# Performance work log

Hardware: AMD Instinct MI355X
Metric: run time of the kernel (lower is better)

The kernel has to match this reference:

```python
import jax, jax.numpy as jnp
import numpy as np

B, S, LC, DIM, H, FFN = 1, 3600, 512, 1536, 12, 8960
HD = DIM // H          # 128
GRID = (4, 30, 30)     # f*h*w == S
K_LEN = 9900           # hardcoded k_lens in SelfAttention.forward
EPS = 1e-6

def _rope_axis_angles(n_pos, dim):
    inv = 1.0 / np.power(10000.0, np.arange(0, dim, 2, dtype=np.float64) / dim)
    return np.outer(np.arange(n_pos), inv)

def _build_rope(grid, head_dim):
    c = head_dim // 2                      # 64
    c1, c2 = c - 2 * (c // 3), c // 3      # 22, 21 (Wan 3D rope split)
    f, h, w = grid
    af = _rope_axis_angles(f, 2 * c1)
    ah = _rope_axis_angles(h, 2 * c2)
    aw = _rope_axis_angles(w, 2 * c2)
    ang = np.concatenate([
        np.broadcast_to(af[:, None, None, :], (f, h, w, c1)),
        np.broadcast_to(ah[None, :, None, :], (f, h, w, c2)),
        np.broadcast_to(aw[None, None, :, :], (f, h, w, c2)),
    ], axis=-1).reshape(f * h * w, c)
    return np.cos(ang).astype(np.float32), np.sin(ang).astype(np.float32)

def setup_inputs():
    key = jax.random.key(0)
    ks = iter(jax.random.split(key, 40))
    cos, sin = _build_rope(GRID, HD)
    inp = {
        'x': jax.random.normal(next(ks), (B, S, DIM), dtype=jnp.float32),
        'context': jax.random.normal(next(ks), (B, LC, DIM), dtype=jnp.float32),
        't_mod': 0.1 * jax.random.normal(next(ks), (B, 6, DIM), dtype=jnp.float32),
        'rope_cos': jnp.asarray(cos), 'rope_sin': jnp.asarray(sin),
        'modulation': jax.random.normal(next(ks), (1, 6, DIM), dtype=jnp.float32) / DIM ** 0.5,
    }
    for p in ('sa', 'ca'):
        for w in ('q', 'k', 'v', 'o'):
            inp[p + '_' + w + 'w'] = 0.02 * jax.random.normal(next(ks), (DIM, DIM), dtype=jnp.float32)
            inp[p + '_' + w + 'b'] = jnp.zeros((DIM,), jnp.float32)
        inp[p + '_nq'] = jnp.ones((DIM,), jnp.float32)
        inp[p + '_nk'] = jnp.ones((DIM,), jnp.float32)
    inp['n3_w'] = jnp.ones((DIM,), jnp.float32)
    inp['n3_b'] = jnp.zeros((DIM,), jnp.float32)
    inp['ffn_w1'] = 0.02 * jax.random.normal(next(ks), (DIM, FFN), dtype=jnp.float32)
    inp['ffn_b1'] = jnp.zeros((FFN,), jnp.float32)
    inp['ffn_w2'] = 0.02 * jax.random.normal(next(ks), (FFN, DIM), dtype=jnp.float32)
    inp['ffn_b2'] = jnp.zeros((DIM,), jnp.float32)
    return inp

def _rms(x, w):
    x32 = x.astype(jnp.float32)
    n = x32 * jax.lax.rsqrt(jnp.mean(x32 * x32, axis=-1, keepdims=True) + EPS)
    return n.astype(x.dtype) * w

def _ln(x, w=None, b=None):
    mu = jnp.mean(x, axis=-1, keepdims=True)
    var = jnp.mean(jnp.square(x - mu), axis=-1, keepdims=True)
    y = (x - mu) * jax.lax.rsqrt(var + EPS)
    return y if w is None else y * w + b

def _rope(x, cos, sin):
    b, s, h, d = x.shape
    x2 = x.reshape(b, s, h, d // 2, 2)
    xe, xo = x2[..., 0], x2[..., 1]
    c, sn = cos[None, :, None, :], sin[None, :, None, :]
    return jnp.stack([xe * c - xo * sn, xe * sn + xo * c], axis=-1).reshape(b, s, h, d)

def _attn(q, k, v, k_len=None):
    # q,k,v: [B,S,H,D]
    scores = jnp.einsum('bqhd,bkhd->bhqk', q, k) * (q.shape[-1] ** -0.5)
    if k_len is not None:
        mask = jnp.arange(k.shape[1]) < k_len
        scores = jnp.where(mask[None, None, None, :], scores, jnp.finfo(scores.dtype).min)
    return jnp.einsum('bhqk,bkhd->bqhd', jax.nn.softmax(scores, axis=-1), v)

def reference(x, context, t_mod, rope_cos, rope_sin, modulation,
              sa_qw, sa_qb, sa_kw, sa_kb, sa_vw, sa_vb, sa_ow, sa_ob, sa_nq, sa_nk,
              ca_qw, ca_qb, ca_kw, ca_kb, ca_vw, ca_vb, ca_ow, ca_ob, ca_nq, ca_nk,
              n3_w, n3_b, ffn_w1, ffn_b1, ffn_w2, ffn_b2):
    mod = modulation + t_mod                      # [B,6,DIM]
    sh_msa, sc_msa, g_msa, sh_mlp, sc_mlp, g_mlp = [mod[:, i:i + 1] for i in range(6)]
    b = x.shape[0]
    # --- self-attention with AdaLN modulate + 3D RoPE + k_lens mask ---
    h = _ln(x) * (1 + sc_msa) + sh_msa
    q = _rms(h @ sa_qw + sa_qb, sa_nq).reshape(b, -1, H, HD)
    k = _rms(h @ sa_kw + sa_kb, sa_nk).reshape(b, -1, H, HD)
    v = (h @ sa_vw + sa_vb).reshape(b, -1, H, HD)
    a = _attn(_rope(q, rope_cos, rope_sin), _rope(k, rope_cos, rope_sin), v, k_len=K_LEN)
    x = x + g_msa * (a.reshape(b, -1, DIM) @ sa_ow + sa_ob)
    # --- cross-attention ---
    hc = _ln(x, n3_w, n3_b)
    q = _rms(hc @ ca_qw + ca_qb, ca_nq).reshape(b, -1, H, HD)
    k = _rms(context @ ca_kw + ca_kb, ca_nk).reshape(b, -1, H, HD)
    v = (context @ ca_vw + ca_vb).reshape(b, -1, H, HD)
    x = x + (_attn(q, k, v).reshape(b, -1, DIM) @ ca_ow + ca_ob)
    # --- gated FFN with AdaLN modulate ---
    h = _ln(x) * (1 + sc_mlp) + sh_mlp
    h = jax.nn.gelu(h @ ffn_w1 + ffn_b1, approximate=True) @ ffn_w2 + ffn_b2
    return x + g_mlp * h
```

## Files before the change

kernel.cpp:

```cpp
#include <hip/hip_runtime.h>
#include <cstdint>

#define S_LEN 3600
#define DMODEL 1536
#define LCTX 512
#define NH 12
#define HDIM 128
#define FFND 8960
#define SPAD_SELF 3648

typedef short v8s __attribute__((ext_vector_type(8)));
typedef float v4f __attribute__((ext_vector_type(4)));
typedef unsigned short u16b;
typedef unsigned int u32b;

#define AS1 __attribute__((address_space(1)))
#define AS3 __attribute__((address_space(3)))

__device__ __forceinline__ void gl_lds16(const void* g, void* l){
  __builtin_amdgcn_global_load_lds((AS1 const void*)g, (AS3 void*)l, 16, 0, 0);
}

__device__ __forceinline__ u16b f2b(float f){
  union { float f; u32b i; } x; x.f = f;
  u32b r = x.i + 0x7fffu + ((x.i >> 16) & 1u);
  return (u16b)(r >> 16);
}

__device__ __forceinline__ u32b cvtpk(float a, float b){
  u32b r;
  asm("v_cvt_pk_bf16_f32 %0, %1, %2" : "=v"(r) : "v"(a), "v"(b));
  return r;
}

__device__ __forceinline__ int swz4(int row){ return (row ^ (row >> 2)) & 3; }

__global__ void add_vec(const float* __restrict__ a, const float* __restrict__ b,
                        float* __restrict__ o, int n){
  int i = blockIdx.x * 256 + threadIdx.x;
  if (i < n) o[i] = a[i] + b[i];
}

__global__ void f2b_kernel(const float* __restrict__ in, u16b* __restrict__ out, int n){
  int i = blockIdx.x * 256 + threadIdx.x;
  if (i < n) out[i] = f2b(in[i]);
}

struct WJob { const float* W; u16b* WT; int K; int N; int t0; };
struct WJobs { WJob j[10]; };

__global__ __launch_bounds__(256) void wconv(WJobs jobs){
  __shared__ float tile[32][33];
  int b = blockIdx.x;
  int ji = 0;
  #pragma unroll
  for (int i = 0; i < 10; ++i) if (b >= jobs.j[i].t0) ji = i;
  WJob jb = jobs.j[ji];
  int rel = b - jb.t0;
  int ntn = jb.N / 32;
  int k0 = (rel / ntn) * 32, n0 = (rel % ntn) * 32;
  int tx = threadIdx.x & 31, ty = threadIdx.x >> 5;
  #pragma unroll
  for (int r = ty; r < 32; r += 8) tile[r][tx] = jb.W[(size_t)(k0 + r) * jb.N + n0 + tx];
  __syncthreads();
  #pragma unroll
  for (int r = ty; r < 32; r += 8) jb.WT[(size_t)(n0 + r) * jb.K + k0 + tx] = f2b(tile[tx][r]);
}

__global__ __launch_bounds__(256) void vtrans(const u16b* __restrict__ V,
                                              u16b* __restrict__ Vt,
                                              int S, int Spad){
  __shared__ u16b t[32][136];
  int h = blockIdx.y, kb = blockIdx.x * 32, tid = threadIdx.x;
  int row = tid >> 3, ch = tid & 7;
  int key = kb + row;
  if (key < S){
    float4 a = *(const float4*)(V + (size_t)key * DMODEL + h * HDIM + ch * 16);
    float4 b = *(const float4*)(V + (size_t)key * DMODEL + h * HDIM + ch * 16 + 8);
    *(float4*)&t[row][ch * 16] = a;
    *(float4*)&t[row][ch * 16 + 8] = b;
  } else {
    float4 z = {0.f, 0.f, 0.f, 0.f};
    *(float4*)&t[row][ch * 16] = z;
    *(float4*)&t[row][ch * 16 + 8] = z;
  }
  __syncthreads();
  int hd = tid >> 1, kc = (tid & 1) * 16;
  u16b* dst = Vt + ((size_t)h * HDIM + hd) * Spad + kb + kc;
  #pragma unroll
  for (int e = 0; e < 16; e += 2){
    u32b pk = ((u32b)t[kc + e][hd]) | (((u32b)t[kc + e + 1][hd]) << 16);
    *(u32b*)(dst + e) = pk;
  }
}

__global__ __launch_bounds__(256) void ln_mod(const float* __restrict__ X,
                                              const float* __restrict__ gamma,
                                              const float* __restrict__ beta,
                                              float gadd, u16b* __restrict__ out){
  int row = blockIdx.x;
  const float* xr = X + (size_t)row * DMODEL;
  int tid = threadIdx.x;
  float v[6]; float s1 = 0.f, s2 = 0.f;
  #pragma unroll
  for (int j = 0; j < 6; ++j){ v[j] = xr[tid + j * 256]; s1 += v[j]; s2 += v[j] * v[j]; }
  #pragma unroll
  for (int o = 1; o < 64; o <<= 1){ s1 += __shfl_xor(s1, o); s2 += __shfl_xor(s2, o); }
  __shared__ float red[8];
  int wid = tid >> 6, lane = tid & 63;
  if (!lane){ red[wid * 2] = s1; red[wid * 2 + 1] = s2; }
  __syncthreads();
  s1 = red[0] + red[2] + red[4] + red[6];
  s2 = red[1] + red[3] + red[5] + red[7];
  float mu = s1 / DMODEL;
  float var = s2 / DMODEL - mu * mu;
  float rstd = rsqrtf(var + 1e-6f);
  #pragma unroll
  for (int j = 0; j < 6; ++j){
    int c = tid + j * 256;
    float g = gamma[c] + gadd;
    float b = beta[c];
    out[(size_t)row * DMODEL + c] = f2b((v[j] - mu) * rstd * g + b);
  }
}

__global__ __launch_bounds__(256) void rms_rope(const float* __restrict__ X,
                                                const float* __restrict__ w,
                                                const float* __restrict__ cosT,
                                                const float* __restrict__ sinT,
                                                float qmul,
                                                u16b* __restrict__ out){
  int row = blockIdx.x;
  const float* xr = X + (size_t)row * DMODEL;
  int tid = threadIdx.x;
  float2 v[3]; float ss = 0.f;
  #pragma unroll
  for (int j = 0; j < 3; ++j){
    v[j] = *(const float2*)(xr + 2 * (tid + j * 256));
    ss += v[j].x * v[j].x + v[j].y * v[j].y;
  }
  #pragma unroll
  for (int o = 1; o < 64; o <<= 1) ss += __shfl_xor(ss, o);
  __shared__ float red[4];
  int wid = tid >> 6, lane = tid & 63;
  if (!lane) red[wid] = ss;
  __syncthreads();
  ss = red[0] + red[1] + red[2] + red[3];
  float rstd = rsqrtf(ss / DMODEL + 1e-6f);
  #pragma unroll
  for (int j = 0; j < 3; ++j){
    int p = tid + j * 256;
    float xe = v[j].x * rstd * w[2 * p];
    float xo = v[j].y * rstd * w[2 * p + 1];
    float oe, oo;
    if (cosT){
      int d = p & 63;
      float c = cosT[row * 64 + d], sn = sinT[row * 64 + d];
      oe = xe * c - xo * sn; oo = xe * sn + xo * c;
    } else { oe = xe; oo = xo; }
    oe *= qmul; oo *= qmul;
    u32b packed = ((u32b)f2b(oe)) | (((u32b)f2b(oo)) << 16);
    *(u32b*)(out + (size_t)row * DMODEL + 2 * p) = packed;
  }
}

template<int EPI>
__global__ __launch_bounds__(256, 2) void gemm_bt(
    const u16b* __restrict__ A, const u16b* __restrict__ BT,
    const float* __restrict__ bias, const float* __restrict__ res,
    const float* __restrict__ gate, float* __restrict__ outF,
    u16b* __restrict__ outB, int M, int N, int K, int kLen)
{
  __shared__ char Asm[2][8192];
  __shared__ char Bsm[2][8192];
  const int tid = threadIdx.x, lane = tid & 63, wid = tid >> 6;
  const int bm = blockIdx.x * 128, bn = blockIdx.y * 128;
  const int kbase = blockIdx.z * kLen;
  const int wm = (wid >> 1) * 64, wn = (wid & 1) * 64;
  v4f acc[4][4] = {};

  auto stage = [&](int buf, int k0){
    #pragma unroll
    for (int c = 0; c < 2; ++c){
      int seg = wid * 2 + c;
      int l = seg * 64 + lane;
      int row = l >> 2, cs = l & 3;
      int col = cs ^ swz4(row);
      gl_lds16(A + (size_t)min(bm + row, M - 1) * K + kbase + k0 + col * 8,
               Asm[buf] + seg * 1024);
      gl_lds16(BT + (size_t)(bn + row) * K + kbase + k0 + col * 8,
               Bsm[buf] + seg * 1024);
    }
  };

  const int nt = kLen / 32;
  int cur = 0;
  stage(0, 0);
  __syncthreads();
  const int chk = lane >> 4, qr = lane & 15;
  for (int t = 0; t < nt; ++t){
    if (t + 1 < nt) stage(cur ^ 1, (t + 1) * 32);
    char* Ab = Asm[cur]; char* Bb = Bsm[cur];
    v8s af[4], bfr[4];
    #pragma unroll
    for (int f = 0; f < 4; ++f){
      int rowa = wm + f * 16 + qr;
      af[f] = *(const v8s*)(Ab + rowa * 64 + ((chk ^ swz4(rowa)) * 16));
      int rowb = wn + f * 16 + qr;
      bfr[f] = *(const v8s*)(Bb + rowb * 64 + ((chk ^ swz4(rowb)) * 16));
    }
    __builtin_amdgcn_s_setprio(1);
    #pragma unroll
    for (int i = 0; i < 4; ++i)
      #pragma unroll
      for (int j = 0; j < 4; ++j)
        acc[i][j] = __builtin_amdgcn_mfma_f32_16x16x32_bf16(af[i], bfr[j], acc[i][j], 0, 0, 0);
    __builtin_amdgcn_s_setprio(0);
    __syncthreads();
    cur ^= 1;
  }
  const int rr = lane >> 4;
  #pragma unroll
  for (int i = 0; i < 4; ++i){
    #pragma unroll
    for (int j = 0; j < 4; ++j){
      int n = bn + wn + j * 16 + qr;
      float bv = (EPI != 5 && bias) ? bias[n] : 0.f;
      float gv = (EPI == 2 && gate) ? gate[n] : 1.f;
      #pragma unroll
      for (int r = 0; r < 4; ++r){
        int m = bm + wm + i * 16 + rr * 4 + r;
        if (m < M){
          float val = acc[i][j][r] + bv;
          size_t idx = (size_t)m * N + n;
          if (EPI == 0) outB[idx] = f2b(val);
          else if (EPI == 1) outF[idx] = val;
          else if (EPI == 2) outF[idx] = res[idx] + gv * val;
          else if (EPI == 5) outF[(size_t)blockIdx.z * M * N + idx] = val;
          else {
            float t3 = val * val * val;
            float th = tanhf(0.7978845608028654f * (val + 0.044715f * t3));
            outB[idx] = f2b(0.5f * val * (1.f + th));
          }
        }
      }
    }
  }
}

struct Seg { const float* bias; float* outF; u16b* outB; };
struct Segs { Seg s[3]; };

__global__ __launch_bounds__(256, 2) void gemm_seg(
    const u16b* __restrict__ A, const u16b* __restrict__ BT,
    Segs segs, int M, int N, int K)
{
  __shared__ char Asm[2][8192];
  __shared__ char Bsm[2][8192];
  const int tid = threadIdx.x, lane = tid & 63, wid = tid >> 6;
  const int bm = blockIdx.x * 128, bn = blockIdx.y * 128;
  const int wm = (wid >> 1) * 64, wn = (wid & 1) * 64;
  v4f acc[4][4] = {};

  auto stage = [&](int buf, int k0){
    #pragma unroll
    for (int c = 0; c < 2; ++c){
      int seg = wid * 2 + c;
      int l = seg * 64 + lane;
      int row = l >> 2, cs = l & 3;
      int col = cs ^ swz4(row);
      gl_lds16(A + (size_t)min(bm + row, M - 1) * K + k0 + col * 8,
               Asm[buf] + seg * 1024);
      gl_lds16(BT + (size_t)(bn + row) * K + k0 + col * 8,
               Bsm[buf] + seg * 1024);
    }
  };

  const int nt = K / 32;
  int cur = 0;
  stage(0, 0);
  __syncthreads();
  const int chk = lane >> 4, qr = lane & 15;
  for (int t = 0; t < nt; ++t){
    if (t + 1 < nt) stage(cur ^ 1, (t + 1) * 32);
    char* Ab = Asm[cur]; char* Bb = Bsm[cur];
    v8s af[4], bfr[4];
    #pragma unroll
    for (int f = 0; f < 4; ++f){
      int rowa = wm + f * 16 + qr;
      af[f] = *(const v8s*)(Ab + rowa * 64 + ((chk ^ swz4(rowa)) * 16));
      int rowb = wn + f * 16 + qr;
      bfr[f] = *(const v8s*)(Bb + rowb * 64 + ((chk ^ swz4(rowb)) * 16));
    }
    __builtin_amdgcn_s_setprio(1);
    #pragma unroll
    for (int i = 0; i < 4; ++i)
      #pragma unroll
      for (int j = 0; j < 4; ++j)
        acc[i][j] = __builtin_amdgcn_mfma_f32_16x16x32_bf16(af[i], bfr[j], acc[i][j], 0, 0, 0);
    __builtin_amdgcn_s_setprio(0);
    __syncthreads();
    cur ^= 1;
  }
  const int seg = bn / 1536;
  const Seg sg = segs.s[seg];
  const int rr = lane >> 4;
  #pragma unroll
  for (int i = 0; i < 4; ++i){
    #pragma unroll
    for (int j = 0; j < 4; ++j){
      int nloc = bn - seg * 1536 + wn + j * 16 + qr;
      float bv = sg.bias[nloc];
      #pragma unroll
      for (int r = 0; r < 4; ++r){
        int m = bm + wm + i * 16 + rr * 4 + r;
        if (m < M){
          float val = acc[i][j][r] + bv;
          size_t idx = (size_t)m * 1536 + nloc;
          if (sg.outB) sg.outB[idx] = f2b(val);
          else sg.outF[idx] = val;
        }
      }
    }
  }
}

__global__ __launch_bounds__(256) void ffn2_reduce(const float* __restrict__ part,
                                                   const float* __restrict__ res,
                                                   const float* __restrict__ bias,
                                                   const float* __restrict__ gate,
                                                   float* __restrict__ out, int total){
  int i4 = blockIdx.x * 256 + threadIdx.x;
  if (i4 * 4 >= total) return;
  int base = i4 * 4;
  int n = base % DMODEL;
  float4 p0 = *(const float4*)(part + base);
  float4 p1 = *(const float4*)(part + (size_t)total + base);
  float4 rs = *(const float4*)(res + base);
  float4 bv = *(const float4*)(bias + n);
  float4 gv = *(const float4*)(gate + n);
  float4 o;
  o.x = rs.x + gv.x * (p0.x + p1.x + bv.x);
  o.y = rs.y + gv.y * (p0.y + p1.y + bv.y);
  o.z = rs.z + gv.z * (p0.z + p1.z + bv.z);
  o.w = rs.w + gv.w * (p0.w + p1.w + bv.w);
  *(float4*)(out + base) = o;
}

__global__ __launch_bounds__(256) void merge_o(const float* __restrict__ op0,
                                               const float* __restrict__ op1,
                                               const float2* __restrict__ ml,
                                               u16b* __restrict__ outO, int Sq){
  int i4 = blockIdx.x * 256 + threadIdx.x;
  const int perRow = DMODEL / 4;
  if (i4 >= Sq * perRow) return;
  int row = i4 / perRow, c4 = (i4 % perRow) * 4;
  int h = c4 >> 7;
  float2 ml0 = ml[h * Sq + row];
  float2 ml1 = ml[NH * Sq + h * Sq + row];
  float M = fmaxf(ml0.x, ml1.x);
  float w0 = exp2f(ml0.x - M), w1 = exp2f(ml1.x - M);
  float inv = 1.f / (ml0.y * w0 + ml1.y * w1);
  float4 a = *(const float4*)(op0 + (size_t)row * DMODEL + c4);
  float4 b = *(const float4*)(op1 + (size_t)row * DMODEL + c4);
  u32b lo = ((u32b)f2b((a.x * w0 + b.x * w1) * inv)) | (((u32b)f2b((a.y * w0 + b.y * w1) * inv)) << 16);
  u32b hi = ((u32b)f2b((a.z * w0 + b.z * w1) * inv)) | (((u32b)f2b((a.w * w0 + b.w * w1) * inv)) << 16);
  uint2 w2; w2.x = lo; w2.y = hi;
  *(uint2*)(outO + (size_t)row * DMODEL + c4) = w2;
}

__global__ __launch_bounds__(256, 4) void flash_attn(
    const u16b* __restrict__ Q, const u16b* __restrict__ Kp,
    const u16b* __restrict__ Vt, u16b* __restrict__ O,
    float* __restrict__ op0, float* __restrict__ op1,
    float2* __restrict__ mlbuf,
    int Sq, int Sk, int ksplit, int Spad)
{
  __shared__ char KV[32768];
  __shared__ char Pall[8192];
  const int tid = threadIdx.x, lane = tid & 63, wid = tid >> 6;
  const int h = blockIdx.y;
  const int z = blockIdx.z;
  const int kbeg = z * ksplit;
  const int kend = min(kbeg + ksplit, Sk);
  const int q0 = blockIdx.x * 64 + wid * 16;
  const int qq = lane & 15, cc = lane >> 4;
  char* Kb = KV; char* Vb = KV + 16384;
  char* Pb = Pall + wid * 2048;

  v8s qf[4];
  {
    int qrow = min(q0 + qq, Sq - 1);
    const u16b* qp = Q + (size_t)qrow * DMODEL + h * HDIM + cc * 8;
    #pragma unroll
    for (int ks = 0; ks < 4; ++ks) qf[ks] = *(const v8s*)(qp + ks * 32);
  }

  auto stage = [&](int kb0){
    #pragma unroll
    for (int c = 0; c < 4; ++c){
      int seg = wid * 4 + c;
      int g = seg * 64 + lane;
      int krow = g >> 4, kcol = (g & 15) ^ (krow & 7);
      gl_lds16(Kp + (size_t)min(kb0 + krow, Sk - 1) * DMODEL + h * HDIM + kcol * 8,
               Kb + seg * 1024);
      int vrow = g >> 3, vcol = (g & 7) ^ (vrow & 7);
      gl_lds16(Vt + ((size_t)h * HDIM + vrow) * Spad + kb0 + vcol * 8,
               Vb + seg * 1024);
    }
  };

  float mrun = -1e30f, lrun = 0.f;
  v4f oacc[8] = {};
  const int nt = (kend - kbeg + 63) >> 6;

  for (int t = 0; t < nt; ++t){
    int kb0 = kbeg + (t << 6);
    stage(kb0);
    __syncthreads();
    v4f sc[4];
    __builtin_amdgcn_s_setprio(1);
    #pragma unroll
    for (int sub = 0; sub < 4; ++sub){
      v4f sa = {0.f, 0.f, 0.f, 0.f};
      int row = sub * 16 + qq;
      #pragma unroll
      for (int ks = 0; ks < 4; ++ks){
        v8s kf = *(const v8s*)(Kb + row * 256 + (((ks * 4 + cc) ^ (row & 7)) * 16));
        sa = __builtin_amdgcn_mfma_f32_16x16x32_bf16(kf, qf[ks], sa, 0, 0, 0);
      }
      sc[sub] = sa;
    }
    __builtin_amdgcn_s_setprio(0);
    if (kb0 + 64 > kend){
      #pragma unroll
      for (int sub = 0; sub < 4; ++sub)
        #pragma unroll
        for (int r = 0; r < 4; ++r)
          if (kb0 + sub * 16 + cc * 4 + r >= kend) sc[sub][r] = -1e30f;
    }
    float m01 = fmaxf(fmaxf(sc[0][0], sc[0][1]), fmaxf(sc[0][2], sc[0][3]));
    float m23 = fmaxf(fmaxf(sc[1][0], sc[1][1]), fmaxf(sc[1][2], sc[1][3]));
    float m45 = fmaxf(fmaxf(sc[2][0], sc[2][1]), fmaxf(sc[2][2], sc[2][3]));
    float m67 = fmaxf(fmaxf(sc[3][0], sc[3][1]), fmaxf(sc[3][2], sc[3][3]));
    float pmax = fmaxf(fmaxf(m01, m23), fmaxf(m45, m67));
    pmax = fmaxf(pmax, __shfl_xor(pmax, 16));
    pmax = fmaxf(pmax, __shfl_xor(pmax, 32));
    if (!__all(pmax <= mrun + 11.54f)){
      float mnew = fmaxf(mrun, pmax);
      float alpha = exp2f(mrun - mnew);
      mrun = mnew;
      float alr[4];
      #pragma unroll
      for (int r = 0; r < 4; ++r) alr[r] = __shfl(alpha, cc * 4 + r);
      #pragma unroll
      for (int f = 0; f < 8; ++f)
        #pragma unroll
        for (int r = 0; r < 4; ++r) oacc[f][r] *= alr[r];
      lrun *= alpha;
    }
    float csum = 0.f;
    #pragma unroll
    for (int sub = 0; sub < 4; ++sub){
      float s0 = 0.f, s1 = 0.f;
      #pragma unroll
      for (int r = 0; r < 4; r += 2){
        float p0 = exp2f(sc[sub][r] - mrun);
        float p1 = exp2f(sc[sub][r + 1] - mrun);
        sc[sub][r] = p0; sc[sub][r + 1] = p1;
        s0 += p0; s1 += p1;
      }
      csum += s0 + s1;
    }
    csum += __shfl_xor(csum, 16);
    csum += __shfl_xor(csum, 32);
    lrun += csum;
    #pragma unroll
    for (int sub = 0; sub < 4; ++sub){
      uint2 w2;
      w2.x = cvtpk(sc[sub][0], sc[sub][1]);
      w2.y = cvtpk(sc[sub][2], sc[sub][3]);
      int gI = sub * 2 + (cc >> 1);
      *(uint2*)(Pb + qq * 128 + ((gI ^ (qq & 7)) * 16) + (cc & 1) * 8) = w2;
    }
    v8s pf0 = *(const v8s*)(Pb + qq * 128 + (((cc) ^ (qq & 7)) * 16));
    v8s pf1 = *(const v8s*)(Pb + qq * 128 + (((4 + cc) ^ (qq & 7)) * 16));
    __builtin_amdgcn_s_setprio(1);
    #pragma unroll
    for (int hdb = 0; hdb < 8; ++hdb){
      int row = hdb * 16 + qq;
      v8s vf0 = *(const v8s*)(Vb + row * 128 + (((cc) ^ (row & 7)) * 16));
      v8s vf1 = *(const v8s*)(Vb + row * 128 + (((4 + cc) ^ (row & 7)) * 16));
      oacc[hdb] = __builtin_amdgcn_mfma_f32_16x16x32_bf16(pf0, vf0, oacc[hdb], 0, 0, 0);
      oacc[hdb] = __builtin_amdgcn_mfma_f32_16x16x32_bf16(pf1, vf1, oacc[hdb], 0, 0, 0);
    }
    __builtin_amdgcn_s_setprio(0);
    __syncthreads();
  }

  if (mlbuf){
    float* op = z ? op1 : op0;
    #pragma unroll
    for (int hdb = 0; hdb < 8; ++hdb)
      #pragma unroll
      for (int r = 0; r < 4; ++r){
        int qrow = q0 + cc * 4 + r;
        if (qrow < Sq)
          op[(size_t)qrow * DMODEL + h * HDIM + hdb * 16 + qq] = oacc[hdb][r];
      }
    if (cc == 0 && q0 + qq < Sq)
      mlbuf[(size_t)z * NH * Sq + (size_t)h * Sq + q0 + qq] = make_float2(mrun, lrun);
  } else {
    float linv = 1.f / lrun;
    float lr[4];
    #pragma unroll
    for (int r = 0; r < 4; ++r) lr[r] = __shfl(linv, cc * 4 + r);
    #pragma unroll
    for (int hdb = 0; hdb < 8; ++hdb)
      #pragma unroll
      for (int r = 0; r < 4; ++r){
        int qrow = q0 + cc * 4 + r;
        if (qrow < Sq)
          O[(size_t)qrow * DMODEL + h * HDIM + hdb * 16 + qq] = f2b(oacc[hdb][r] * lr[r]);
      }
  }
}

extern "C" void kernel_launch(void* const* d_in, const int* in_sizes, int n_in,
                              void* d_out, int out_size, void* d_ws, size_t ws_size,
                              hipStream_t stream){
  (void)in_sizes; (void)n_in; (void)out_size; (void)ws_size;
  const float* x     = (const float*)d_in[0];
  const float* ctx   = (const float*)d_in[1];
  const float* t_mod = (const float*)d_in[2];
  const float* ropec = (const float*)d_in[3];
  const float* ropes = (const float*)d_in[4];
  const float* modu  = (const float*)d_in[5];
  const float* sa_qw = (const float*)d_in[6];  const float* sa_qb = (const float*)d_in[7];
  const float* sa_kw = (const float*)d_in[8];  const float* sa_kb = (const float*)d_in[9];
  const float* sa_vw = (const float*)d_in[10]; const float* sa_vb = (const float*)d_in[11];
  const float* sa_ow = (const float*)d_in[12]; const float* sa_ob = (const float*)d_in[13];
  const float* sa_nq = (const float*)d_in[14]; const float* sa_nk = (const float*)d_in[15];
  const float* ca_qw = (const float*)d_in[16]; const float* ca_qb = (const float*)d_in[17];
  const float* ca_kw = (const float*)d_in[18]; const float* ca_kb = (const float*)d_in[19];
  const float* ca_vw = (const float*)d_in[20]; const float* ca_vb = (const float*)d_in[21];
  const float* ca_ow = (const float*)d_in[22]; const float* ca_ob = (const float*)d_in[23];
  const float* ca_nq = (const float*)d_in[24]; const float* ca_nk = (const float*)d_in[25];
  const float* n3w   = (const float*)d_in[26]; const float* n3b   = (const float*)d_in[27];
  const float* fw1   = (const float*)d_in[28]; const float* fb1   = (const float*)d_in[29];
  const float* fw2   = (const float*)d_in[30]; const float* fb2   = (const float*)d_in[31];
  float* out = (float*)d_out;

  const float QSCALE = 0.08838834764831845f * 1.4426950408889634f;

  char* wsp = (char*)d_ws;
  size_t off = 0;
  auto alloc = [&](size_t b){ void* p = wsp + off; off += (b + 255) & ~(size_t)255; return p; };
  const size_t WW = (size_t)DMODEL * DMODEL * 2;
  float* modc = (float*)alloc(6 * DMODEL * 4);
  u16b* w1T   = (u16b*)alloc((size_t)FFND * DMODEL * 2);
  u16b* w2T   = (u16b*)alloc((size_t)DMODEL * FFND * 2);
  u16b* h_bf  = (u16b*)alloc((size_t)S_LEN * DMODEL * 2);
  float* pre0 = (float*)alloc((size_t)S_LEN * DMODEL * 4);
  size_t region0 = off;
  u16b* sa_qkvT = (u16b*)alloc(3 * WW);
  u16b* sa_owT  = (u16b*)alloc(WW);
  u16b* ca_qwT  = (u16b*)alloc(WW);
  u16b* ca_kvT  = (u16b*)alloc(2 * WW);
  u16b* ca_owT  = (u16b*)alloc(WW);
  float* x2    = (float*)alloc((size_t)S_LEN * DMODEL * 4);
  float* pre2  = (float*)alloc((size_t)LCTX * DMODEL * 4);
  u16b* qb     = (u16b*)alloc((size_t)S_LEN * DMODEL * 2);
  u16b* kb     = (u16b*)alloc((size_t)S_LEN * DMODEL * 2);
  u16b* vb     = (u16b*)alloc((size_t)S_LEN * DMODEL * 2);
  u16b* ab     = (u16b*)alloc((size_t)S_LEN * DMODEL * 2);
  u16b* ctxb   = (u16b*)alloc((size_t)LCTX * DMODEL * 2);
  u16b* k2b    = (u16b*)alloc((size_t)LCTX * DMODEL * 2);
  u16b* v2b    = (u16b*)alloc((size_t)LCTX * DMODEL * 2);
  u16b* vts    = (u16b*)alloc((size_t)NH * HDIM * SPAD_SELF * 2);
  u16b* vtc    = (u16b*)alloc((size_t)NH * HDIM * LCTX * 2);
  u16b* fmid = (u16b*)(wsp + region0);
  float* fpart = (float*)(wsp + region0 + (size_t)S_LEN * FFND * 2);

  add_vec<<<36, 256, 0, stream>>>(modu, t_mod, modc, 6 * DMODEL);

  WJobs jobs; int t = 0;
  auto addjob = [&](int i, const float* w_, u16b* wt, int K, int N){
    jobs.j[i].W = w_; jobs.j[i].WT = wt; jobs.j[i].K = K; jobs.j[i].N = N; jobs.j[i].t0 = t;
    t += (K / 32) * (N / 32);
  };
  addjob(0, sa_qw, sa_qkvT, DMODEL, DMODEL);
  addjob(1, sa_kw, sa_qkvT + (size_t)DMODEL * DMODEL, DMODEL, DMODEL);
  addjob(2, sa_vw, sa_qkvT + (size_t)2 * DMODEL * DMODEL, DMODEL, DMODEL);
  addjob(3, sa_ow, sa_owT, DMODEL, DMODEL);
  addjob(4, ca_qw, ca_qwT, DMODEL, DMODEL);
  addjob(5, ca_kw, ca_kvT, DMODEL, DMODEL);
  addjob(6, ca_vw, ca_kvT + (size_t)DMODEL * DMODEL, DMODEL, DMODEL);
  addjob(7, ca_ow, ca_owT, DMODEL, DMODEL);
  addjob(8, fw1, w1T, DMODEL, FFND);
  addjob(9, fw2, w2T, FFND, DMODEL);
  wconv<<<t, 256, 0, stream>>>(jobs);

  f2b_kernel<<<(LCTX * DMODEL) / 256, 256, 0, stream>>>(ctx, ctxb, LCTX * DMODEL);

  ln_mod<<<S_LEN, 256, 0, stream>>>(x, modc + DMODEL, modc, 1.f, h_bf);
  dim3 g12(29, 12);
  {
    Segs sg;
    sg.s[0] = { sa_qb, pre0, nullptr };
    sg.s[1] = { sa_kb, x2,   nullptr };
    sg.s[2] = { sa_vb, nullptr, vb   };
    gemm_seg<<<dim3(29, 36), 256, 0, stream>>>(h_bf, sa_qkvT, sg, S_LEN, 3 * DMODEL, DMODEL);
  }
  rms_rope<<<S_LEN, 256, 0, stream>>>(pre0, sa_nq, ropec, ropes, QSCALE, qb);
  rms_rope<<<S_LEN, 256, 0, stream>>>(x2, sa_nk, ropec, ropes, 1.f, kb);
  vtrans<<<dim3(SPAD_SELF / 32, 12), 256, 0, stream>>>(vb, vts, S_LEN, SPAD_SELF);
  flash_attn<<<dim3(57, 12, 2), 256, 0, stream>>>(qb, kb, vts, ab,
      (float*)pre0, (float*)x2, (float2*)vb, S_LEN, S_LEN, 1856, SPAD_SELF);
  merge_o<<<(S_LEN * (DMODEL / 4) + 255) / 256, 256, 0, stream>>>(
      (const float*)pre0, (const float*)x2, (const float2*)vb, ab, S_LEN);
  gemm_bt<2><<<g12, 256, 0, stream>>>(ab, sa_owT, sa_ob, x, modc + 2 * DMODEL, x2, nullptr, S_LEN, DMODEL, DMODEL, DMODEL);

  ln_mod<<<S_LEN, 256, 0, stream>>>(x2, n3w, n3b, 0.f, h_bf);
  gemm_bt<1><<<g12, 256, 0, stream>>>(h_bf, ca_qwT, ca_qb, nullptr, nullptr, pre0, nullptr, S_LEN, DMODEL, DMODEL, DMODEL);
  {
    Segs sg;
    sg.s[0] = { ca_kb, pre2, nullptr };
    sg.s[1] = { ca_vb, nullptr, v2b  };
    sg.s[2] = { ca_vb, nullptr, v2b  };
    gemm_seg<<<dim3(4, 24), 256, 0, stream>>>(ctxb, ca_kvT, sg, LCTX, 2 * DMODEL, DMODEL);
  }
  rms_rope<<<S_LEN, 256, 0, stream>>>(pre0, ca_nq, nullptr, nullptr, QSCALE, qb);
  rms_rope<<<LCTX, 256, 0, stream>>>(pre2, ca_nk, nullptr, nullptr, 1.f, k2b);
  vtrans<<<dim3(16, 12), 256, 0, stream>>>(v2b, vtc, LCTX, LCTX);
  flash_attn<<<dim3(57, 12, 2), 256, 0, stream>>>(qb, k2b, vtc, ab,
      (float*)pre0, (float*)kb, (float2*)vts, S_LEN, LCTX, 256, LCTX);
  merge_o<<<(S_LEN * (DMODEL / 4) + 255) / 256, 256, 0, stream>>>(
      (const float*)pre0, (const float*)kb, (const float2*)vts, ab, S_LEN);
  gemm_bt<2><<<g12, 256, 0, stream>>>(ab, ca_owT, ca_ob, x2, nullptr, pre0, nullptr, S_LEN, DMODEL, DMODEL, DMODEL);

  ln_mod<<<S_LEN, 256, 0, stream>>>(pre0, modc + 4 * DMODEL, modc + 3 * DMODEL, 1.f, h_bf);
  gemm_bt<3><<<dim3(29, 70), 256, 0, stream>>>(h_bf, w1T, fb1, nullptr, nullptr, nullptr, fmid, S_LEN, FFND, DMODEL, DMODEL);
  gemm_bt<5><<<dim3(29, 12, 2), 256, 0, stream>>>(fmid, w2T, nullptr, nullptr, nullptr, fpart, nullptr, S_LEN, DMODEL, FFND, FFND / 2);
  ffn2_reduce<<<(S_LEN * DMODEL / 4 + 255) / 256, 256, 0, stream>>>(fpart, pre0, fb2, modc + 5 * DMODEL, out, S_LEN * DMODEL);
}
```

Before: 1.008 ms.

## Add 256x256 tiled GEMM with XCD swizzle for QKV and FFN GEMMs

```diff
diff --git a/kernel.cpp b/kernel.cpp
--- a/kernel.cpp
+++ b/kernel.cpp
@@ -34,6 +34,12 @@
 }
 
 __device__ __forceinline__ int swz4(int row){ return (row ^ (row >> 2)) & 3; }
+
+__device__ __forceinline__ int xcd_swz(int orig, int nwg){
+  int q8 = nwg >> 3, r8 = nwg & 7;
+  int xcd = orig & 7, idx = orig >> 3;
+  return (xcd < r8 ? xcd * (q8 + 1) : r8 * (q8 + 1) + (xcd - r8) * q8) + idx;
+}
 
 __global__ void add_vec(const float* __restrict__ a, const float* __restrict__ b,
                         float* __restrict__ o, int n){
@@ -164,6 +170,116 @@
   }
 }
 
+struct Seg { const float* bias; float* outF; u16b* outB; };
+struct Segs { Seg s[3]; };
+
+template<int EPI>
+__global__ __launch_bounds__(512, 2) void gemm256(
+    const u16b* __restrict__ A, const u16b* __restrict__ BT,
+    Segs segs, const float* __restrict__ bias,
+    float* __restrict__ outF, u16b* __restrict__ outB,
+    int M, int N, int K, int kLen, int nxM)
+{
+  __shared__ char Abuf[2][32768];
+  __shared__ char Bbuf[2][32768];
+  const int tid = threadIdx.x, lane = tid & 63, wid = tid >> 6;
+  const int nwg = gridDim.x;
+  const int swz = xcd_swz(blockIdx.x, nwg);
+  const int bx = swz % nxM;
+  const int byz = swz / nxM;
+  const int nyN = N / 256;
+  const int by = (EPI == 2) ? (byz % nyN) : byz;
+  const int z  = (EPI == 2) ? (byz / nyN) : 0;
+  const int bm = bx * 256, bn = by * 256;
+  const int kbase = z * kLen;
+  const int wm = (wid >> 2) * 128, wn = (wid & 3) * 64;
+  const int qr = lane & 15, chk = lane >> 4;
+  v4f acc[8][4] = {};
+
+  auto stageT = [&](int buf, int t){
+    int k0 = kbase + t * 64;
+    #pragma unroll
+    for (int c = 0; c < 4; ++c){
+      int l = c * 512 + tid;
+      int row = l >> 3, g = l & 7;
+      int col = (g ^ (row & 7)) * 8;
+      gl_lds16(A + (size_t)min(bm + row, M - 1) * K + k0 + col, Abuf[buf] + l * 16);
+      gl_lds16(BT + (size_t)(bn + row) * K + k0 + col, Bbuf[buf] + l * 16);
+    }
+  };
+
+  const int nt = kLen / 64;
+  int cur = 0;
+  stageT(0, 0);
+  __syncthreads();
+  for (int t = 0; t < nt; ++t){
+    if (t + 1 < nt) stageT(cur ^ 1, t + 1);
+    char* Ab = Abuf[cur]; char* Bb = Bbuf[cur];
+    v8s bf2[4][2];
+    #pragma unroll
+    for (int fc = 0; fc < 4; ++fc)
+      #pragma unroll
+      for (int kk = 0; kk < 2; ++kk){
+        int row = wn + fc * 16 + qr;
+        bf2[fc][kk] = *(const v8s*)(Bb + row * 128 + (((kk * 4 + chk) ^ (row & 7)) * 16));
+      }
+    #pragma unroll
+    for (int p = 0; p < 4; ++p){
+      int r0 = wm + p * 32 + qr;
+      int r1 = r0 + 16;
+      v8s a0[2], a1[2];
+      #pragma unroll
+      for (int kk = 0; kk < 2; ++kk){
+        a0[kk] = *(const v8s*)(Ab + r0 * 128 + (((kk * 4 + chk) ^ (r0 & 7)) * 16));
+        a1[kk] = *(const v8s*)(Ab + r1 * 128 + (((kk * 4 + chk) ^ (r1 & 7)) * 16));
+      }
+      __builtin_amdgcn_s_setprio(1);
+      #pragma unroll
+      for (int kk = 0; kk < 2; ++kk)
+        #pragma unroll
+        for (int fc = 0; fc < 4; ++fc){
+          acc[p * 2][fc]     = __builtin_amdgcn_mfma_f32_16x16x32_bf16(a0[kk], bf2[fc][kk], acc[p * 2][fc], 0, 0, 0);
+          acc[p * 2 + 1][fc] = __builtin_amdgcn_mfma_f32_16x16x32_bf16(a1[kk], bf2[fc][kk], acc[p * 2 + 1][fc], 0, 0, 0);
+        }
+      __builtin_amdgcn_s_setprio(0);
+    }
+    __syncthreads();
+    cur ^= 1;
+  }
+
+  const int rr = lane >> 4;
+  const int sgi = (EPI == 0) ? (bn / 1536) : 0;
+  #pragma unroll
+  for (int fr = 0; fr < 8; ++fr){
+    #pragma unroll
+    for (int fc = 0; fc < 4; ++fc){
+      int n = bn + wn + fc * 16 + qr;
+      #pragma unroll
+      for (int r = 0; r < 4; ++r){
+        int m = bm + wm + fr * 16 + rr * 4 + r;
+        if (m < M){
+          float val = acc[fr][fc][r];
+          if (EPI == 0){
+            Seg sg = segs.s[sgi];
+            int nloc = n - sgi * 1536;
+            float v2 = val + sg.bias[nloc];
+            size_t idx = (size_t)m * 1536 + nloc;
+            if (sg.outB) sg.outB[idx] = f2b(v2);
+            else sg.outF[idx] = v2;
+          } else if (EPI == 1){
+            float v2 = val + bias[n];
+            float t3 = v2 * v2 * v2;
+            float g = v2 / (1.f + __expf(-1.5957691216057308f * (v2 + 0.044715f * t3)));
+            outB[(size_t)m * N + n] = f2b(g);
+          } else {
+            outF[(size_t)z * M * 1536 + (size_t)m * 1536 + n] = val;
+          }
+        }
+      }
+    }
+  }
+}
+
 template<int EPI>
 __global__ __launch_bounds__(256, 2) void gemm_bt(
     const u16b* __restrict__ A, const u16b* __restrict__ BT,
@@ -174,7 +290,9 @@
   __shared__ char Asm[2][8192];
   __shared__ char Bsm[2][8192];
   const int tid = threadIdx.x, lane = tid & 63, wid = tid >> 6;
-  const int bm = blockIdx.x * 128, bn = blockIdx.y * 128;
+  const int nwg = gridDim.x * gridDim.y;
+  const int swz = xcd_swz(blockIdx.x + gridDim.x * blockIdx.y, nwg);
+  const int bm = (swz % gridDim.x) * 128, bn = (swz / gridDim.x) * 128;
   const int kbase = blockIdx.z * kLen;
   const int wm = (wid >> 1) * 64, wn = (wid & 1) * 64;
   v4f acc[4][4] = {};
@@ -225,7 +343,7 @@
     #pragma unroll
     for (int j = 0; j < 4; ++j){
       int n = bn + wn + j * 16 + qr;
-      float bv = (EPI != 5 && bias) ? bias[n] : 0.f;
+      float bv = bias ? bias[n] : 0.f;
       float gv = (EPI == 2 && gate) ? gate[n] : 1.f;
       #pragma unroll
       for (int r = 0; r < 4; ++r){
@@ -233,23 +351,13 @@
         if (m < M){
           float val = acc[i][j][r] + bv;
           size_t idx = (size_t)m * N + n;
-          if (EPI == 0) outB[idx] = f2b(val);
-          else if (EPI == 1) outF[idx] = val;
-          else if (EPI == 2) outF[idx] = res[idx] + gv * val;
-          else if (EPI == 5) outF[(size_t)blockIdx.z * M * N + idx] = val;
-          else {
-            float t3 = val * val * val;
-            float th = tanhf(0.7978845608028654f * (val + 0.044715f * t3));
-            outB[idx] = f2b(0.5f * val * (1.f + th));
-          }
+          if (EPI == 1) outF[idx] = val;
+          else outF[idx] = res[idx] + gv * val;
         }
       }
     }
   }
 }
-
-struct Seg { const float* bias; float* outF; u16b* outB; };
-struct Segs { Seg s[3]; };
 
 __global__ __launch_bounds__(256, 2) void gemm_seg(
     const u16b* __restrict__ A, const u16b* __restrict__ BT,
@@ -258,7 +366,9 @@
   __shared__ char Asm[2][8192];
   __shared__ char Bsm[2][8192];
   const int tid = threadIdx.x, lane = tid & 63, wid = tid >> 6;
-  const int bm = blockIdx.x * 128, bn = blockIdx.y * 128;
+  const int nwg = gridDim.x * gridDim.y;
+  const int swz = xcd_swz(blockIdx.x + gridDim.x * blockIdx.y, nwg);
+  const int bm = (swz % gridDim.x) * 128, bn = (swz / gridDim.x) * 128;
   const int wm = (wid >> 1) * 64, wn = (wid & 1) * 64;
   v4f acc[4][4] = {};
 
@@ -603,6 +713,8 @@
 
   f2b_kernel<<<(LCTX * DMODEL) / 256, 256, 0, stream>>>(ctx, ctxb, LCTX * DMODEL);
 
+  Segs dummy = {};
+
   ln_mod<<<S_LEN, 256, 0, stream>>>(x, modc + DMODEL, modc, 1.f, h_bf);
   dim3 g12(29, 12);
   {
@@ -610,7 +722,8 @@
     sg.s[0] = { sa_qb, pre0, nullptr };
     sg.s[1] = { sa_kb, x2,   nullptr };
     sg.s[2] = { sa_vb, nullptr, vb   };
-    gemm_seg<<<dim3(29, 36), 256, 0, stream>>>(h_bf, sa_qkvT, sg, S_LEN, 3 * DMODEL, DMODEL);
+    gemm256<0><<<15 * 18, 512, 0, stream>>>(h_bf, sa_qkvT, sg, nullptr, nullptr, nullptr,
+                                            S_LEN, 3 * DMODEL, DMODEL, DMODEL, 15);
   }
   rms_rope<<<S_LEN, 256, 0, stream>>>(pre0, sa_nq, ropec, ropes, QSCALE, qb);
   rms_rope<<<S_LEN, 256, 0, stream>>>(x2, sa_nk, ropec, ropes, 1.f, kb);
@@ -640,7 +753,9 @@
   gemm_bt<2><<<g12, 256, 0, stream>>>(ab, ca_owT, ca_ob, x2, nullptr, pre0, nullptr, S_LEN, DMODEL, DMODEL, DMODEL);
 
   ln_mod<<<S_LEN, 256, 0, stream>>>(pre0, modc + 4 * DMODEL, modc + 3 * DMODEL, 1.f, h_bf);
-  gemm_bt<3><<<dim3(29, 70), 256, 0, stream>>>(h_bf, w1T, fb1, nullptr, nullptr, nullptr, fmid, S_LEN, FFND, DMODEL, DMODEL);
-  gemm_bt<5><<<dim3(29, 12, 2), 256, 0, stream>>>(fmid, w2T, nullptr, nullptr, nullptr, fpart, nullptr, S_LEN, DMODEL, FFND, FFND / 2);
+  gemm256<1><<<15 * 35, 512, 0, stream>>>(h_bf, w1T, dummy, fb1, nullptr, fmid,
+                                          S_LEN, FFND, DMODEL, DMODEL, 15);
+  gemm256<2><<<15 * 6 * 2, 512, 0, stream>>>(fmid, w2T, dummy, nullptr, fpart, nullptr,
+                                             S_LEN, DMODEL, FFND, FFND / 2, 15);
   ffn2_reduce<<<(S_LEN * DMODEL / 4 + 255) / 256, 256, 0, stream>>>(fpart, pre0, fb2, modc + 5 * DMODEL, out, S_LEN * DMODEL);
 }
```

Measured after the change: 1.126 ms. +11.7%, slower.

## Triple-buffer GEMM LDS pipeline, add XCD swizzle, raise FFN2 split-K to four

Applied to the files above, without the earlier changes.

```diff
diff --git a/kernel.cpp b/kernel.cpp
--- a/kernel.cpp
+++ b/kernel.cpp
@@ -34,6 +34,12 @@
 }
 
 __device__ __forceinline__ int swz4(int row){ return (row ^ (row >> 2)) & 3; }
+
+__device__ __forceinline__ int xcd_swz(int orig, int nwg){
+  int q8 = nwg >> 3, r8 = nwg & 7;
+  int xcd = orig & 7, idx = orig >> 3;
+  return (xcd < r8 ? xcd * (q8 + 1) : r8 * (q8 + 1) + (xcd - r8) * q8) + idx;
+}
 
 __global__ void add_vec(const float* __restrict__ a, const float* __restrict__ b,
                         float* __restrict__ o, int n){
@@ -164,6 +170,9 @@
   }
 }
 
+struct Seg { const float* bias; float* outF; u16b* outB; };
+struct Segs { Seg s[3]; };
+
 template<int EPI>
 __global__ __launch_bounds__(256, 2) void gemm_bt(
     const u16b* __restrict__ A, const u16b* __restrict__ BT,
@@ -171,98 +180,17 @@
     const float* __restrict__ gate, float* __restrict__ outF,
     u16b* __restrict__ outB, int M, int N, int K, int kLen)
 {
-  __shared__ char Asm[2][8192];
-  __shared__ char Bsm[2][8192];
+  __shared__ char Ls[3][16384];
   const int tid = threadIdx.x, lane = tid & 63, wid = tid >> 6;
-  const int bm = blockIdx.x * 128, bn = blockIdx.y * 128;
+  const int nwg = gridDim.x * gridDim.y;
+  const int swz = xcd_swz(blockIdx.x + gridDim.x * blockIdx.y, nwg);
+  const int bm = (swz % gridDim.x) * 128, bn = (swz / gridDim.x) * 128;
   const int kbase = blockIdx.z * kLen;
   const int wm = (wid >> 1) * 64, wn = (wid & 1) * 64;
   v4f acc[4][4] = {};
 
-  auto stage = [&](int buf, int k0){
-    #pragma unroll
-    for (int c = 0; c < 2; ++c){
-      int seg = wid * 2 + c;
-      int l = seg * 64 + lane;
-      int row = l >> 2, cs = l & 3;
-      int col = cs ^ swz4(row);
-      gl_lds16(A + (size_t)min(bm + row, M - 1) * K + kbase + k0 + col * 8,
-               Asm[buf] + seg * 1024);
-      gl_lds16(BT + (size_t)(bn + row) * K + kbase + k0 + col * 8,
-               Bsm[buf] + seg * 1024);
-    }
-  };
-
-  const int nt = kLen / 32;
-  int cur = 0;
-  stage(0, 0);
-  __syncthreads();
-  const int chk = lane >> 4, qr = lane & 15;
-  for (int t = 0; t < nt; ++t){
-    if (t + 1 < nt) stage(cur ^ 1, (t + 1) * 32);
-    char* Ab = Asm[cur]; char* Bb = Bsm[cur];
-    v8s af[4], bfr[4];
-    #pragma unroll
-    for (int f = 0; f < 4; ++f){
-      int rowa = wm + f * 16 + qr;
-      af[f] = *(const v8s*)(Ab + rowa * 64 + ((chk ^ swz4(rowa)) * 16));
-      int rowb = wn + f * 16 + qr;
-      bfr[f] = *(const v8s*)(Bb + rowb * 64 + ((chk ^ swz4(rowb)) * 16));
-    }
-    __builtin_amdgcn_s_setprio(1);
-    #pragma unroll
-    for (int i = 0; i < 4; ++i)
-      #pragma unroll
-      for (int j = 0; j < 4; ++j)
-        acc[i][j] = __builtin_amdgcn_mfma_f32_16x16x32_bf16(af[i], bfr[j], acc[i][j], 0, 0, 0);
-    __builtin_amdgcn_s_setprio(0);
-    __syncthreads();
-    cur ^= 1;
-  }
-  const int rr = lane >> 4;
-  #pragma unroll
-  for (int i = 0; i < 4; ++i){
-    #pragma unroll
-    for (int j = 0; j < 4; ++j){
-      int n = bn + wn + j * 16 + qr;
-      float bv = (EPI != 5 && bias) ? bias[n] : 0.f;
-      float gv = (EPI == 2 && gate) ? gate[n] : 1.f;
-      #pragma unroll
-      for (int r = 0; r < 4; ++r){
-        int m = bm + wm + i * 16 + rr * 4 + r;
-        if (m < M){
-          float val = acc[i][j][r] + bv;
-          size_t idx = (size_t)m * N + n;
-          if (EPI == 0) outB[idx] = f2b(val);
-          else if (EPI == 1) outF[idx] = val;
-          else if (EPI == 2) outF[idx] = res[idx] + gv * val;
-          else if (EPI == 5) outF[(size_t)blockIdx.z * M * N + idx] = val;
-          else {
-            float t3 = val * val * val;
-            float th = tanhf(0.7978845608028654f * (val + 0.044715f * t3));
-            outB[idx] = f2b(0.5f * val * (1.f + th));
-          }
-        }
-      }
-    }
-  }
-}
-
-struct Seg { const float* bias; float* outF; u16b* outB; };
-struct Segs { Seg s[3]; };
-
-__global__ __launch_bounds__(256, 2) void gemm_seg(
-    const u16b* __restrict__ A, const u16b* __restrict__ BT,
-    Segs segs, int M, int N, int K)
-{
-  __shared__ char Asm[2][8192];
-  __shared__ char Bsm[2][8192];
-  const int tid = threadIdx.x, lane = tid & 63, wid = tid >> 6;
-  const int bm = blockIdx.x * 128, bn = blockIdx.y * 128;
-  const int wm = (wid >> 1) * 64, wn = (wid & 1) * 64;
-  v4f acc[4][4] = {};
-
-  auto stage = [&](int buf, int k0){
+  auto stage = [&](int buf, int t){
+    int k0 = kbase + t * 32;
     #pragma unroll
     for (int c = 0; c < 2; ++c){
       int seg = wid * 2 + c;
@@ -270,20 +198,22 @@
       int row = l >> 2, cs = l & 3;
       int col = cs ^ swz4(row);
       gl_lds16(A + (size_t)min(bm + row, M - 1) * K + k0 + col * 8,
-               Asm[buf] + seg * 1024);
+               Ls[buf] + seg * 1024);
       gl_lds16(BT + (size_t)(bn + row) * K + k0 + col * 8,
-               Bsm[buf] + seg * 1024);
+               Ls[buf] + 8192 + seg * 1024);
     }
   };
 
-  const int nt = K / 32;
-  int cur = 0;
+  const int nt = kLen / 32;
   stage(0, 0);
-  __syncthreads();
+  stage(1, 1);
   const int chk = lane >> 4, qr = lane & 15;
   for (int t = 0; t < nt; ++t){
-    if (t + 1 < nt) stage(cur ^ 1, (t + 1) * 32);
-    char* Ab = Asm[cur]; char* Bb = Bsm[cur];
+    if (t + 1 < nt) asm volatile("s_waitcnt vmcnt(4)" ::: "memory");
+    else            asm volatile("s_waitcnt vmcnt(0)" ::: "memory");
+    __builtin_amdgcn_s_barrier();
+    if (t + 2 < nt) stage((t + 2) % 3, t + 2);
+    char* Ab = Ls[t % 3]; char* Bb = Ab + 8192;
     v8s af[4], bfr[4];
     #pragma unroll
     for (int f = 0; f < 4; ++f){
@@ -299,8 +229,87 @@
       for (int j = 0; j < 4; ++j)
         acc[i][j] = __builtin_amdgcn_mfma_f32_16x16x32_bf16(af[i], bfr[j], acc[i][j], 0, 0, 0);
     __builtin_amdgcn_s_setprio(0);
-    __syncthreads();
-    cur ^= 1;
+  }
+  const int rr = lane >> 4;
+  #pragma unroll
+  for (int i = 0; i < 4; ++i){
+    #pragma unroll
+    for (int j = 0; j < 4; ++j){
+      int n = bn + wn + j * 16 + qr;
+      float bv = (EPI != 5 && bias) ? bias[n] : 0.f;
+      float gv = (EPI == 2 && gate) ? gate[n] : 1.f;
+      #pragma unroll
+      for (int r = 0; r < 4; ++r){
+        int m = bm + wm + i * 16 + rr * 4 + r;
+        if (m < M){
+          float val = acc[i][j][r] + bv;
+          size_t idx = (size_t)m * N + n;
+          if (EPI == 1) outF[idx] = val;
+          else if (EPI == 2) outF[idx] = res[idx] + gv * val;
+          else if (EPI == 5) outF[(size_t)blockIdx.z * M * N + idx] = val;
+          else {
+            float t3 = val * val * val;
+            float g = val / (1.f + __expf(-1.5957691216057308f * (val + 0.044715f * t3)));
+            outB[idx] = f2b(g);
+          }
+        }
+      }
+    }
+  }
+}
+
+__global__ __launch_bounds__(256, 2) void gemm_seg(
+    const u16b* __restrict__ A, const u16b* __restrict__ BT,
+    Segs segs, int M, int N, int K)
+{
+  __shared__ char Ls[3][16384];
+  const int tid = threadIdx.x, lane = tid & 63, wid = tid >> 6;
+  const int nwg = gridDim.x * gridDim.y;
+  const int swz = xcd_swz(blockIdx.x + gridDim.x * blockIdx.y, nwg);
+  const int bm = (swz % gridDim.x) * 128, bn = (swz / gridDim.x) * 128;
+  const int wm = (wid >> 1) * 64, wn = (wid & 1) * 64;
+  v4f acc[4][4] = {};
+
+  auto stage = [&](int buf, int t){
+    int k0 = t * 32;
+    #pragma unroll
+    for (int c = 0; c < 2; ++c){
+      int seg = wid * 2 + c;
+      int l = seg * 64 + lane;
+      int row = l >> 2, cs = l & 3;
+      int col = cs ^ swz4(row);
+      gl_lds16(A + (size_t)min(bm + row, M - 1) * K + k0 + col * 8,
+               Ls[buf] + seg * 1024);
+      gl_lds16(BT + (size_t)(bn + row) * K + k0 + col * 8,
+               Ls[buf] + 8192 + seg * 1024);
+    }
+  };
+
+  const int nt = K / 32;
+  stage(0, 0);
+  stage(1, 1);
+  const int chk = lane >> 4, qr = lane & 15;
+  for (int t = 0; t < nt; ++t){
+    if (t + 1 < nt) asm volatile("s_waitcnt vmcnt(4)" ::: "memory");
+    else            asm volatile("s_waitcnt vmcnt(0)" ::: "memory");
+    __builtin_amdgcn_s_barrier();
+    if (t + 2 < nt) stage((t + 2) % 3, t + 2);
+    char* Ab = Ls[t % 3]; char* Bb = Ab + 8192;
+    v8s af[4], bfr[4];
+    #pragma unroll
+    for (int f = 0; f < 4; ++f){
+      int rowa = wm + f * 16 + qr;
+      af[f] = *(const v8s*)(Ab + rowa * 64 + ((chk ^ swz4(rowa)) * 16));
+      int rowb = wn + f * 16 + qr;
+      bfr[f] = *(const v8s*)(Bb + rowb * 64 + ((chk ^ swz4(rowb)) * 16));
+    }
+    __builtin_amdgcn_s_setprio(1);
+    #pragma unroll
+    for (int i = 0; i < 4; ++i)
+      #pragma unroll
+      for (int j = 0; j < 4; ++j)
+        acc[i][j] = __builtin_amdgcn_mfma_f32_16x16x32_bf16(af[i], bfr[j], acc[i][j], 0, 0, 0);
+    __builtin_amdgcn_s_setprio(0);
   }
   const int seg = bn / 1536;
   const Seg sg = segs.s[seg];
@@ -336,14 +345,16 @@
   int n = base % DMODEL;
   float4 p0 = *(const float4*)(part + base);
   float4 p1 = *(const float4*)(part + (size_t)total + base);
+  float4 p2 = *(const float4*)(part + 2 * (size_t)total + base);
+  float4 p3 = *(const float4*)(part + 3 * (size_t)total + base);
   float4 rs = *(const float4*)(res + base);
   float4 bv = *(const float4*)(bias + n);
   float4 gv = *(const float4*)(gate + n);
   float4 o;
-  o.x = rs.x + gv.x * (p0.x + p1.x + bv.x);
-  o.y = rs.y + gv.y * (p0.y + p1.y + bv.y);
-  o.z = rs.z + gv.z * (p0.z + p1.z + bv.z);
-  o.w = rs.w + gv.w * (p0.w + p1.w + bv.w);
+  o.x = rs.x + gv.x * (p0.x + p1.x + p2.x + p3.x + bv.x);
+  o.y = rs.y + gv.y * (p0.y + p1.y + p2.y + p3.y + bv.y);
+  o.z = rs.z + gv.z * (p0.z + p1.z + p2.z + p3.z + bv.z);
+  o.w = rs.w + gv.w * (p0.w + p1.w + p2.w + p3.w + bv.w);
   *(float4*)(out + base) = o;
 }
 
@@ -641,6 +652,6 @@
 
   ln_mod<<<S_LEN, 256, 0, stream>>>(pre0, modc + 4 * DMODEL, modc + 3 * DMODEL, 1.f, h_bf);
   gemm_bt<3><<<dim3(29, 70), 256, 0, stream>>>(h_bf, w1T, fb1, nullptr, nullptr, nullptr, fmid, S_LEN, FFND, DMODEL, DMODEL);
-  gemm_bt<5><<<dim3(29, 12, 2), 256, 0, stream>>>(fmid, w2T, nullptr, nullptr, nullptr, fpart, nullptr, S_LEN, DMODEL, FFND, FFND / 2);
+  gemm_bt<5><<<dim3(29, 12, 4), 256, 0, stream>>>(fmid, w2T, nullptr, nullptr, nullptr, fpart, nullptr, S_LEN, DMODEL, FFND, FFND / 4);
   ffn2_reduce<<<(S_LEN * DMODEL / 4 + 255) / 256, 256, 0, stream>>>(fpart, pre0, fb2, modc + 5 * DMODEL, out, S_LEN * DMODEL);
 }
```

Result: faster. 964.5 us (-4.3%).
